# Kernel tuning notes

Measured on AMD Instinct MI355X. Metric: run time of the kernel, lower is better.

The kernel has to match this reference:

```python
import jax, jax.numpy as jnp
import numpy as np

B, E, D, H, A = 65536, 16, 256, 64, 18  # batch, n_subpolicies, emb_dim, hidden, n_actions


def setup_inputs() -> dict:
    key = jax.random.key(0)
    ks = jax.random.split(key, 16)
    s = lambda k, sh: jax.random.normal(k, sh, dtype=jnp.float32) * 0.05
    return dict(
        obs=s(ks[0], (B, D)),
        h=s(ks[1], (B, D)),
        c=s(ks[2], (B, D)),
        idxs=jax.random.randint(ks[3], (B,), 0, E, dtype=jnp.int32),
        # Observer: LSTMCell(D, D) params (torch layout: [4D, D] with i,f,g,o gate order)
        W_ih=s(ks[4], (4 * D, D)), W_hh=s(ks[5], (4 * D, D)),
        b_ih=s(ks[6], (4 * D,)), b_hh=s(ks[7], (4 * D,)),
        # Stacked SubPolicy actor params: Linear(D,64)-Tanh-Linear(64,A)
        Wa1=s(ks[8], (E, D, H)), ba1=s(ks[9], (E, H)),
        Wa2=s(ks[10], (E, H, A)), ba2=s(ks[11], (E, A)),
        # Stacked SubPolicy critic params: Linear(D,64)-Tanh-Linear(64,1)
        Wc1=s(ks[12], (E, D, H)), bc1=s(ks[13], (E, H)),
        Wc2=s(ks[14], (E, H, 1)), bc2=s(ks[15], (E, 1)),
    )


def reference(obs, h, c, idxs, W_ih, W_hh, b_ih, b_hh,
              Wa1, ba1, Wa2, ba2, Wc1, bc1, Wc2, bc2):
    # ---- Observer: single LSTMCell step ----
    gates = obs @ W_ih.T + b_ih + h @ W_hh.T + b_hh          # [B, 4D]
    gi, gf, gg, go = jnp.split(gates, 4, axis=1)
    i = jax.nn.sigmoid(gi); f = jax.nn.sigmoid(gf); o = jax.nn.sigmoid(go)
    c_new = f * c + i * jnp.tanh(gg)                          # [B, D]
    h_new = o * jnp.tanh(c_new)                               # [B, D]

    # ---- Expert dispatch: evaluate all tiny subpolicy MLPs, select per sample ----
    # (mathematically identical to the per-sample routing loop in forward_sub)
    ha = jnp.tanh(jnp.einsum('bd,edh->beh', h_new, Wa1) + ba1)        # [B, E, H]
    logits_all = jnp.einsum('beh,eha->bea', ha, Wa2) + ba2            # [B, E, A]
    hc = jnp.tanh(jnp.einsum('bd,edh->beh', h_new, Wc1) + bc1)        # [B, E, H]
    vals_all = (jnp.einsum('beh,eho->beo', hc, Wc2) + bc2)[..., 0]    # [B, E]

    b = jnp.arange(h_new.shape[0])
    logits = logits_all[b, idxs]                                       # [B, A]
    values = vals_all[b, idxs]                                         # [B]
    return (h_new, c_new, logits, values)
```

## Files before the change

kernel.cpp:

```cpp
#include <hip/hip_runtime.h>
#include <hip/hip_bf16.h>
#include <math.h>

#define NB 65536
#define ND 256
#define NE 16
#define NH 64
#define NA 18

typedef __bf16 bf16;
typedef __bf16 bf16x4 __attribute__((ext_vector_type(4)));
typedef __bf16 bf16x8 __attribute__((ext_vector_type(8)));
typedef float  f32x4  __attribute__((ext_vector_type(4)));

#define OFF_WCAT 0u
#define OFF_BCAT 1048576u
#define OFF_PW1  1052672u
#define OFF_B1   2101248u
#define OFF_CUR  2109440u
#define OFF_PERM 2109504u

__device__ __forceinline__ float rcp_(float x) { return __builtin_amdgcn_rcpf(x); }
__device__ __forceinline__ float sigm_(float x) {
    return rcp_(1.f + __expf(-x));
}
__device__ __forceinline__ float tanh_(float x) {
    float cl = fminf(fmaxf(x, -15.f), 15.f);
    float e = __expf(2.f * cl);
    return (e - 1.f) * rcp_(e + 1.f);
}

__global__ void k_prep1(const float* __restrict__ W_ih, const float* __restrict__ W_hh,
                        const float* __restrict__ b_ih, const float* __restrict__ b_hh,
                        char* __restrict__ ws) {
    int t = blockIdx.x * 256 + threadIdx.x;
    bf16* Wcat = (bf16*)(ws + OFF_WCAT);
    int kc = t & 63, col = t >> 6;
    int k = kc * 8;
    const float* src = (k < 256) ? (W_ih + (size_t)col * 256 + k)
                                 : (W_hh + (size_t)col * 256 + (k - 256));
    float4 v0 = *(const float4*)(src);
    float4 v1 = *(const float4*)(src + 4);
    bf16x8 o;
    o[0] = (bf16)v0.x; o[1] = (bf16)v0.y; o[2] = (bf16)v0.z; o[3] = (bf16)v0.w;
    o[4] = (bf16)v1.x; o[5] = (bf16)v1.y; o[6] = (bf16)v1.z; o[7] = (bf16)v1.w;
    *(bf16x8*)(Wcat + ((size_t)kc * 1024 + col) * 8) = o;
    if (t < 1024) ((float*)(ws + OFF_BCAT))[t] = b_ih[t] + b_hh[t];
    if (t < 16)   ((int*)(ws + OFF_CUR))[t] = t * 65536;
}

__global__ void k_prep2(const float* __restrict__ Wa1, const float* __restrict__ Wc1,
                        const float* __restrict__ ba1, const float* __restrict__ bc1,
                        char* __restrict__ ws) {
    int t = blockIdx.x * 256 + threadIdx.x;
    bf16* PW1 = (bf16*)(ws + OFF_PW1);
    int col = t & 127, kc = (t >> 7) & 31, e = t >> 12;
    bf16x8 o;
#pragma unroll
    for (int j = 0; j < 8; ++j) {
        int k = kc * 8 + j;
        float v = (col < 64) ? Wa1[((size_t)e * 256 + k) * 64 + col]
                             : Wc1[((size_t)e * 256 + k) * 64 + (col - 64)];
        o[j] = (bf16)v;
    }
    *(bf16x8*)(PW1 + (((size_t)e * 32 + kc) * 128 + col) * 8) = o;
    if (t < 2048) {
        int e2 = t >> 7, c = t & 127;
        ((float*)(ws + OFF_B1))[t] = (c < 64) ? ba1[e2 * 64 + c] : bc1[e2 * 64 + (c - 64)];
    }
}

__global__ void k_scatter(const int* __restrict__ idxs, char* __restrict__ ws) {
    __shared__ int lh[16], lbase[16];
    int t = threadIdx.x;
    int i = blockIdx.x * 256 + t;
    if (t < 16) lh[t] = 0;
    __syncthreads();
    int e = idxs[i];
    int r = atomicAdd(&lh[e], 1);
    __syncthreads();
    int* cur = (int*)(ws + OFF_CUR);
    if (t < 16) lbase[t] = atomicAdd(&cur[t], lh[t]);
    __syncthreads();
    ((int*)(ws + OFF_PERM))[lbase[e] + r] = i;
}

__global__ __launch_bounds__(512, 4) void k_lstm(
    const float* __restrict__ obs, const float* __restrict__ hin,
    const float* __restrict__ cin, const float* __restrict__ bcat,
    const bf16* __restrict__ Wcat,
    float* __restrict__ hout, float* __restrict__ cout) {
    __shared__ alignas(16) char Alds[65536];
    const int tid  = threadIdx.x;
    const int wave = tid >> 6, lane = tid & 63;
    const int lr = lane & 15, lk = lane >> 4;
    const int rb = blockIdx.x & 1023, chalf = blockIdx.x >> 10;
    const int row0 = rb * 64;
    const int colc = chalf * 128 + wave * 16 + lr;

    {
        int sr = tid >> 3, j = tid & 7;
        const float* baseO = obs + (size_t)(row0 + sr) * 256;
        const float* baseH = hin + (size_t)(row0 + sr) * 256;
#pragma unroll
        for (int s = 0; s < 8; ++s) {
            int kc = s * 8 + j;
            const float* sp = (s < 4) ? (baseO + kc * 8) : (baseH + (kc - 32) * 8);
            float4 v0 = *(const float4*)sp;
            float4 v1 = *(const float4*)(sp + 4);
            bf16x8 o;
            o[0] = (bf16)v0.x; o[1] = (bf16)v0.y; o[2] = (bf16)v0.z; o[3] = (bf16)v0.w;
            o[4] = (bf16)v1.x; o[5] = (bf16)v1.y; o[6] = (bf16)v1.z; o[7] = (bf16)v1.w;
            *(bf16x8*)(Alds + kc * 1024 + (((sr ^ (kc & 7))) * 16)) = o;
        }
    }
    __syncthreads();

    int offE[4], offO[4];
#pragma unroll
    for (int m = 0; m < 4; ++m) {
        int R = m * 16 + lr;
        offE[m] = lk * 1024 + ((R ^ lk) * 16);
        offO[m] = lk * 1024 + ((R ^ (lk + 4)) * 16);
    }

    f32x4 acc[4][4];
#pragma unroll
    for (int m = 0; m < 4; ++m)
#pragma unroll
        for (int g = 0; g < 4; ++g)
#pragma unroll
            for (int r = 0; r < 4; ++r) acc[m][g][r] = 0.f;

    const bf16* pB = Wcat + ((size_t)lk * 1024 + colc) * 8;

#pragma unroll
    for (int kf = 0; kf < 16; ++kf) {
        const char* Ab = Alds + kf * 4096;
        bf16x8 a0, a1, a2, a3;
        if (kf & 1) {
            a0 = *(const bf16x8*)(Ab + offO[0]);
            a1 = *(const bf16x8*)(Ab + offO[1]);
            a2 = *(const bf16x8*)(Ab + offO[2]);
            a3 = *(const bf16x8*)(Ab + offO[3]);
        } else {
            a0 = *(const bf16x8*)(Ab + offE[0]);
            a1 = *(const bf16x8*)(Ab + offE[1]);
            a2 = *(const bf16x8*)(Ab + offE[2]);
            a3 = *(const bf16x8*)(Ab + offE[3]);
        }
        const bf16* pBk = pB + (size_t)kf * 4 * 1024 * 8;
        bf16x8 b0 = *(const bf16x8*)(pBk);
        bf16x8 b1 = *(const bf16x8*)(pBk + 256 * 8);
        bf16x8 b2 = *(const bf16x8*)(pBk + 512 * 8);
        bf16x8 b3 = *(const bf16x8*)(pBk + 768 * 8);
        acc[0][0] = __builtin_amdgcn_mfma_f32_16x16x32_bf16(a0, b0, acc[0][0], 0, 0, 0);
        acc[0][1] = __builtin_amdgcn_mfma_f32_16x16x32_bf16(a0, b1, acc[0][1], 0, 0, 0);
        acc[0][2] = __builtin_amdgcn_mfma_f32_16x16x32_bf16(a0, b2, acc[0][2], 0, 0, 0);
        acc[0][3] = __builtin_amdgcn_mfma_f32_16x16x32_bf16(a0, b3, acc[0][3], 0, 0, 0);
        acc[1][0] = __builtin_amdgcn_mfma_f32_16x16x32_bf16(a1, b0, acc[1][0], 0, 0, 0);
        acc[1][1] = __builtin_amdgcn_mfma_f32_16x16x32_bf16(a1, b1, acc[1][1], 0, 0, 0);
        acc[1][2] = __builtin_amdgcn_mfma_f32_16x16x32_bf16(a1, b2, acc[1][2], 0, 0, 0);
        acc[1][3] = __builtin_amdgcn_mfma_f32_16x16x32_bf16(a1, b3, acc[1][3], 0, 0, 0);
        acc[2][0] = __builtin_amdgcn_mfma_f32_16x16x32_bf16(a2, b0, acc[2][0], 0, 0, 0);
        acc[2][1] = __builtin_amdgcn_mfma_f32_16x16x32_bf16(a2, b1, acc[2][1], 0, 0, 0);
        acc[2][2] = __builtin_amdgcn_mfma_f32_16x16x32_bf16(a2, b2, acc[2][2], 0, 0, 0);
        acc[2][3] = __builtin_amdgcn_mfma_f32_16x16x32_bf16(a2, b3, acc[2][3], 0, 0, 0);
        acc[3][0] = __builtin_amdgcn_mfma_f32_16x16x32_bf16(a3, b0, acc[3][0], 0, 0, 0);
        acc[3][1] = __builtin_amdgcn_mfma_f32_16x16x32_bf16(a3, b1, acc[3][1], 0, 0, 0);
        acc[3][2] = __builtin_amdgcn_mfma_f32_16x16x32_bf16(a3, b2, acc[3][2], 0, 0, 0);
        acc[3][3] = __builtin_amdgcn_mfma_f32_16x16x32_bf16(a3, b3, acc[3][3], 0, 0, 0);
    }

    float bi = bcat[colc], bf_ = bcat[256 + colc], bg = bcat[512 + colc], bo = bcat[768 + colc];
#pragma unroll
    for (int m = 0; m < 4; ++m) {
#pragma unroll
        for (int r = 0; r < 4; ++r) {
            int row = row0 + m * 16 + lk * 4 + r;
            float gi = acc[m][0][r] + bi;
            float gf = acc[m][1][r] + bf_;
            float gg = acc[m][2][r] + bg;
            float go = acc[m][3][r] + bo;
            float iv = sigm_(gi), fv = sigm_(gf), gv = tanh_(gg), ov = sigm_(go);
            float co = cin[(size_t)row * 256 + colc];
            float cn = fv * co + iv * gv;
            float hn = ov * tanh_(cn);
            cout[(size_t)row * 256 + colc] = cn;
            hout[(size_t)row * 256 + colc] = hn;
        }
    }
}

__global__ __launch_bounds__(256) void k_expert(
    const float* __restrict__ Wa2, const float* __restrict__ ba2,
    const float* __restrict__ Wc2, const float* __restrict__ bc2,
    char* __restrict__ ws, const float* __restrict__ hsrc,
    float* __restrict__ lout, float* __restrict__ vout) {
    const int e = blockIdx.y;
    const int* cur = (const int*)(ws + OFF_CUR);
    int cnt = cur[e] - e * 65536;
    int r0 = blockIdx.x * 64;
    if (r0 >= cnt) return;
    int nr = min(64, cnt - r0);
    const int* permE = (const int*)(ws + OFF_PERM) + (size_t)e * 65536 + r0;

    __shared__ int rows_s[64];
    __shared__ alignas(16) char smem[128 * 66 * 4];
    bf16*  Alds = (bf16*)smem;
    float* haF  = (float*)smem;

    int t = threadIdx.x;
    if (t < 64) rows_s[t] = permE[(t < nr) ? t : 0];
    __syncthreads();

    {
        int rowi = t >> 2, q = t & 3;
        const float* hp = hsrc + (size_t)rows_s[rowi] * 256;
#pragma unroll
        for (int s = 0; s < 8; ++s) {
            int kc = s * 4 + q;
            float4 v0 = *(const float4*)(hp + kc * 8);
            float4 v1 = *(const float4*)(hp + kc * 8 + 4);
            bf16x8 o;
            o[0] = (bf16)v0.x; o[1] = (bf16)v0.y; o[2] = (bf16)v0.z; o[3] = (bf16)v0.w;
            o[4] = (bf16)v1.x; o[5] = (bf16)v1.y; o[6] = (bf16)v1.z; o[7] = (bf16)v1.w;
            *(bf16x8*)(Alds + ((size_t)kc * 64 + rowi) * 8) = o;
        }
    }
    __syncthreads();

    const bf16* PW1 = (const bf16*)(ws + OFF_PW1) + (size_t)e * 32 * 128 * 8;
    const float* b1 = (const float*)(ws + OFF_B1) + e * 128;
    int wave = t >> 6, lane = t & 63, lr = lane & 15, lk = lane >> 4;

    f32x4 acc[4][2];
#pragma unroll
    for (int m = 0; m < 4; ++m)
#pragma unroll
        for (int n = 0; n < 2; ++n)
#pragma unroll
            for (int r = 0; r < 4; ++r) acc[m][n][r] = 0.f;

#pragma unroll
    for (int kf = 0; kf < 8; ++kf) {
        bf16x8 a[4], bb[2];
#pragma unroll
        for (int m = 0; m < 4; ++m)
            a[m] = *(const bf16x8*)(Alds + (((kf * 4 + lk) * 64) + (m * 16 + lr)) * 8);
#pragma unroll
        for (int n = 0; n < 2; ++n) {
            int colh = wave * 32 + n * 16 + lr;
            int kc = kf * 4 + lk;
            bb[n] = *(const bf16x8*)(PW1 + ((size_t)kc * 128 + colh) * 8);
        }
#pragma unroll
        for (int m = 0; m < 4; ++m)
#pragma unroll
            for (int n = 0; n < 2; ++n)
                acc[m][n] = __builtin_amdgcn_mfma_f32_16x16x32_bf16(a[m], bb[n], acc[m][n], 0, 0, 0);
    }
    __syncthreads();

#pragma unroll
    for (int m = 0; m < 4; ++m)
#pragma unroll
        for (int n = 0; n < 2; ++n) {
            int colh = wave * 32 + n * 16 + lr;
            float bbv = b1[colh];
#pragma unroll
            for (int r = 0; r < 4; ++r) {
                int row = m * 16 + lk * 4 + r;
                haF[colh * 66 + row] = tanh_(acc[m][n][r] + bbv);
            }
        }
    __syncthreads();

    int row = t & 63;
    int grow = rows_s[row];
    bool valid = row < nr;
#pragma unroll
    for (int p = 0; p < 5; ++p) {
        int aI = p * 4 + (t >> 6);
        if (aI < NA) {
            float s = ba2[e * NA + aI];
            for (int hh = 0; hh < 64; ++hh)
                s += haF[hh * 66 + row] * Wa2[((size_t)e * 64 + hh) * NA + aI];
            if (valid) lout[(size_t)grow * NA + aI] = s;
        }
    }
    if (t < 64) {
        float s = bc2[e];
        for (int hh = 0; hh < 64; ++hh)
            s += haF[(64 + hh) * 66 + row] * Wc2[e * 64 + hh];
        if (valid) vout[grow] = s;
    }
}

extern "C" void kernel_launch(void* const* d_in, const int* in_sizes, int n_in,
                              void* d_out, int out_size, void* d_ws, size_t ws_size,
                              hipStream_t stream) {
    const float* obs  = (const float*)d_in[0];
    const float* h    = (const float*)d_in[1];
    const float* c    = (const float*)d_in[2];
    const int*   idxs = (const int*)d_in[3];
    const float* W_ih = (const float*)d_in[4];
    const float* W_hh = (const float*)d_in[5];
    const float* b_ih = (const float*)d_in[6];
    const float* b_hh = (const float*)d_in[7];
    const float* Wa1  = (const float*)d_in[8];
    const float* ba1  = (const float*)d_in[9];
    const float* Wa2  = (const float*)d_in[10];
    const float* ba2  = (const float*)d_in[11];
    const float* Wc1  = (const float*)d_in[12];
    const float* bc1  = (const float*)d_in[13];
    const float* Wc2  = (const float*)d_in[14];
    const float* bc2  = (const float*)d_in[15];

    float* out  = (float*)d_out;
    float* hout = out;
    float* cout = out + (size_t)NB * ND;
    float* lout = out + (size_t)2 * NB * ND;
    float* vout = lout + (size_t)NB * NA;
    char* ws = (char*)d_ws;

    k_prep1<<<dim3(256), dim3(256), 0, stream>>>(W_ih, W_hh, b_ih, b_hh, ws);
    k_prep2<<<dim3(256), dim3(256), 0, stream>>>(Wa1, Wc1, ba1, bc1, ws);
    k_scatter<<<dim3(256), dim3(256), 0, stream>>>(idxs, ws);
    k_lstm<<<dim3(2048), dim3(512), 0, stream>>>(
        obs, h, c, (const float*)(ws + OFF_BCAT), (const bf16*)(ws + OFF_WCAT), hout, cout);
    k_expert<<<dim3(1024, 16), dim3(256), 0, stream>>>(
        Wa2, ba2, Wc2, bc2, ws, hout, lout, vout);
}
```

Baseline: 211.2 us.

## Compute all 1024 gate columns per LSTM block and double-buffer B loads

The LSTM kernel now has each 64-row block compute all 256 hidden columns (1024 gate outputs) instead of splitting columns across two blocks. This halves the grid and avoids staging and converting the obs/h rows to bf16 twice. Each wave now holds 32 accumulators for 8 column tiles, and the weight fragments for the next k-step are prefetched into a second register buffer. Launch bounds drop to 2 blocks per CU to fit the larger register footprint, which cuts occupancy.

```diff
diff --git a/kernel.cpp b/kernel.cpp
--- a/kernel.cpp
+++ b/kernel.cpp
@@ -85,7 +85,7 @@
     ((int*)(ws + OFF_PERM))[lbase[e] + r] = i;
 }
 
-__global__ __launch_bounds__(512, 4) void k_lstm(
+__global__ __launch_bounds__(512, 2) void k_lstm(
     const float* __restrict__ obs, const float* __restrict__ hin,
     const float* __restrict__ cin, const float* __restrict__ bcat,
     const bf16* __restrict__ Wcat,
@@ -94,9 +94,7 @@
     const int tid  = threadIdx.x;
     const int wave = tid >> 6, lane = tid & 63;
     const int lr = lane & 15, lk = lane >> 4;
-    const int rb = blockIdx.x & 1023, chalf = blockIdx.x >> 10;
-    const int row0 = rb * 64;
-    const int colc = chalf * 128 + wave * 16 + lr;
+    const int row0 = blockIdx.x * 64;
 
     {
         int sr = tid >> 3, j = tid & 7;
@@ -124,70 +122,79 @@
         offO[m] = lk * 1024 + ((R ^ (lk + 4)) * 16);
     }
 
-    f32x4 acc[4][4];
+    f32x4 acc[4][8];
 #pragma unroll
     for (int m = 0; m < 4; ++m)
 #pragma unroll
-        for (int g = 0; g < 4; ++g)
-#pragma unroll
-            for (int r = 0; r < 4; ++r) acc[m][g][r] = 0.f;
-
-    const bf16* pB = Wcat + ((size_t)lk * 1024 + colc) * 8;
-
-#pragma unroll
-    for (int kf = 0; kf < 16; ++kf) {
-        const char* Ab = Alds + kf * 4096;
-        bf16x8 a0, a1, a2, a3;
-        if (kf & 1) {
-            a0 = *(const bf16x8*)(Ab + offO[0]);
-            a1 = *(const bf16x8*)(Ab + offO[1]);
-            a2 = *(const bf16x8*)(Ab + offO[2]);
-            a3 = *(const bf16x8*)(Ab + offO[3]);
-        } else {
-            a0 = *(const bf16x8*)(Ab + offE[0]);
-            a1 = *(const bf16x8*)(Ab + offE[1]);
-            a2 = *(const bf16x8*)(Ab + offE[2]);
-            a3 = *(const bf16x8*)(Ab + offE[3]);
-        }
-        const bf16* pBk = pB + (size_t)kf * 4 * 1024 * 8;
-        bf16x8 b0 = *(const bf16x8*)(pBk);
-        bf16x8 b1 = *(const bf16x8*)(pBk + 256 * 8);
-        bf16x8 b2 = *(const bf16x8*)(pBk + 512 * 8);
-        bf16x8 b3 = *(const bf16x8*)(pBk + 768 * 8);
-        acc[0][0] = __builtin_amdgcn_mfma_f32_16x16x32_bf16(a0, b0, acc[0][0], 0, 0, 0);
-        acc[0][1] = __builtin_amdgcn_mfma_f32_16x16x32_bf16(a0, b1, acc[0][1], 0, 0, 0);
-        acc[0][2] = __builtin_amdgcn_mfma_f32_16x16x32_bf16(a0, b2, acc[0][2], 0, 0, 0);
-        acc[0][3] = __builtin_amdgcn_mfma_f32_16x16x32_bf16(a0, b3, acc[0][3], 0, 0, 0);
-        acc[1][0] = __builtin_amdgcn_mfma_f32_16x16x32_bf16(a1, b0, acc[1][0], 0, 0, 0);
-        acc[1][1] = __builtin_amdgcn_mfma_f32_16x16x32_bf16(a1, b1, acc[1][1], 0, 0, 0);
-        acc[1][2] = __builtin_amdgcn_mfma_f32_16x16x32_bf16(a1, b2, acc[1][2], 0, 0, 0);
-        acc[1][3] = __builtin_amdgcn_mfma_f32_16x16x32_bf16(a1, b3, acc[1][3], 0, 0, 0);
-        acc[2][0] = __builtin_amdgcn_mfma_f32_16x16x32_bf16(a2, b0, acc[2][0], 0, 0, 0);
-        acc[2][1] = __builtin_amdgcn_mfma_f32_16x16x32_bf16(a2, b1, acc[2][1], 0, 0, 0);
-        acc[2][2] = __builtin_amdgcn_mfma_f32_16x16x32_bf16(a2, b2, acc[2][2], 0, 0, 0);
-        acc[2][3] = __builtin_amdgcn_mfma_f32_16x16x32_bf16(a2, b3, acc[2][3], 0, 0, 0);
-        acc[3][0] = __builtin_amdgcn_mfma_f32_16x16x32_bf16(a3, b0, acc[3][0], 0, 0, 0);
-        acc[3][1] = __builtin_amdgcn_mfma_f32_16x16x32_bf16(a3, b1, acc[3][1], 0, 0, 0);
-        acc[3][2] = __builtin_amdgcn_mfma_f32_16x16x32_bf16(a3, b2, acc[3][2], 0, 0, 0);
-        acc[3][3] = __builtin_amdgcn_mfma_f32_16x16x32_bf16(a3, b3, acc[3][3], 0, 0, 0);
-    }
-
-    float bi = bcat[colc], bf_ = bcat[256 + colc], bg = bcat[512 + colc], bo = bcat[768 + colc];
-#pragma unroll
-    for (int m = 0; m < 4; ++m) {
-#pragma unroll
-        for (int r = 0; r < 4; ++r) {
-            int row = row0 + m * 16 + lk * 4 + r;
-            float gi = acc[m][0][r] + bi;
-            float gf = acc[m][1][r] + bf_;
-            float gg = acc[m][2][r] + bg;
-            float go = acc[m][3][r] + bo;
-            float iv = sigm_(gi), fv = sigm_(gf), gv = tanh_(gg), ov = sigm_(go);
-            float co = cin[(size_t)row * 256 + colc];
-            float cn = fv * co + iv * gv;
-            float hn = ov * tanh_(cn);
-            cout[(size_t)row * 256 + colc] = cn;
-            hout[(size_t)row * 256 + colc] = hn;
+        for (int n = 0; n < 8; ++n)
+#pragma unroll
+            for (int r = 0; r < 4; ++r) acc[m][n][r] = 0.f;
+
+    const bf16* pB = Wcat + ((size_t)lk * 1024 + wave * 32 + lr) * 8;
+#define BOFF(g, j) ((g) * 2048 + (j) * 128)
+
+    bf16x8 B0[8], B1[8];
+#define LOADB(dst, kf)                                                        \
+    {                                                                         \
+        const bf16* p_ = pB + (size_t)(kf) * 32768;                           \
+        dst[0] = *(const bf16x8*)(p_ + BOFF(0, 0));                           \
+        dst[1] = *(const bf16x8*)(p_ + BOFF(0, 1));                           \
+        dst[2] = *(const bf16x8*)(p_ + BOFF(1, 0));                           \
+        dst[3] = *(const bf16x8*)(p_ + BOFF(1, 1));                           \
+        dst[4] = *(const bf16x8*)(p_ + BOFF(2, 0));                           \
+        dst[5] = *(const bf16x8*)(p_ + BOFF(2, 1));                           \
+        dst[6] = *(const bf16x8*)(p_ + BOFF(3, 0));                           \
+        dst[7] = *(const bf16x8*)(p_ + BOFF(3, 1));                           \
+    }
+
+#define STEP(kf, BCUR, BNXT, OFFA)                                            \
+    {                                                                         \
+        if ((kf) < 15) LOADB(BNXT, (kf) + 1);                                 \
+        const char* Ab_ = Alds + (kf) * 4096;                                 \
+        bf16x8 a0 = *(const bf16x8*)(Ab_ + OFFA[0]);                          \
+        bf16x8 a1 = *(const bf16x8*)(Ab_ + OFFA[1]);                          \
+        bf16x8 a2 = *(const bf16x8*)(Ab_ + OFFA[2]);                          \
+        bf16x8 a3 = *(const bf16x8*)(Ab_ + OFFA[3]);                          \
+        _Pragma("unroll")                                                     \
+        for (int n = 0; n < 8; ++n) {                                         \
+            acc[0][n] = __builtin_amdgcn_mfma_f32_16x16x32_bf16(a0, BCUR[n], acc[0][n], 0, 0, 0); \
+            acc[1][n] = __builtin_amdgcn_mfma_f32_16x16x32_bf16(a1, BCUR[n], acc[1][n], 0, 0, 0); \
+            acc[2][n] = __builtin_amdgcn_mfma_f32_16x16x32_bf16(a2, BCUR[n], acc[2][n], 0, 0, 0); \
+            acc[3][n] = __builtin_amdgcn_mfma_f32_16x16x32_bf16(a3, BCUR[n], acc[3][n], 0, 0, 0); \
+        }                                                                     \
+    }
+
+    LOADB(B0, 0);
+#pragma unroll
+    for (int kk = 0; kk < 8; ++kk) {
+        STEP(kk * 2,     B0, B1, offE);
+        STEP(kk * 2 + 1, B1, B0, offO);
+    }
+#undef STEP
+#undef LOADB
+#undef BOFF
+
+    const int colb = wave * 32 + lr;
+#pragma unroll
+    for (int j = 0; j < 2; ++j) {
+        int col = colb + j * 16;
+        float bi = bcat[col], bf_ = bcat[256 + col], bg = bcat[512 + col], bo = bcat[768 + col];
+#pragma unroll
+        for (int m = 0; m < 4; ++m) {
+#pragma unroll
+            for (int r = 0; r < 4; ++r) {
+                int row = row0 + m * 16 + lk * 4 + r;
+                float gi = acc[m][0 * 2 + j][r] + bi;
+                float gf = acc[m][1 * 2 + j][r] + bf_;
+                float gg = acc[m][2 * 2 + j][r] + bg;
+                float go = acc[m][3 * 2 + j][r] + bo;
+                float iv = sigm_(gi), fv = sigm_(gf), gv = tanh_(gg), ov = sigm_(go);
+                float co = cin[(size_t)row * 256 + col];
+                float cn = fv * co + iv * gv;
+                float hn = ov * tanh_(cn);
+                cout[(size_t)row * 256 + col] = cn;
+                hout[(size_t)row * 256 + col] = hn;
+            }
         }
     }
 }
@@ -327,7 +334,7 @@
     k_prep1<<<dim3(256), dim3(256), 0, stream>>>(W_ih, W_hh, b_ih, b_hh, ws);
     k_prep2<<<dim3(256), dim3(256), 0, stream>>>(Wa1, Wc1, ba1, bc1, ws);
     k_scatter<<<dim3(256), dim3(256), 0, stream>>>(idxs, ws);
-    k_lstm<<<dim3(2048), dim3(512), 0, stream>>>(
+    k_lstm<<<dim3(1024), dim3(512), 0, stream>>>(
         obs, h, c, (const float*)(ws + OFF_BCAT), (const bf16*)(ws + OFF_WCAT), hout, cout);
     k_expert<<<dim3(1024, 16), dim3(256), 0, stream>>>(
         Wa2, ba2, Wc2, bc2, ws, hout, lout, vout);
```

After: 286.6 us. 35.7% more time.

## Double-buffer LSTM GEMM K-loop with direct global-to-LDS weight staging

Applied to the files above, without the earlier changes.

Rewrites the LSTM gate GEMM so that it streams K in eight steps through double-buffered LDS. Weight tiles are staged with global_load_lds into a pre-tiled layout, which k_prep1 now produces, and the next activation tile is loaded and converted while the current one is computed. Blocks shrink to 256 threads covering 64 gate columns, which doubles the grid, and the c input is prefetched during the last step. The goal is to overlap the global loads with the MFMAs and cut per-block LDS use, at the cost of reading the activations once per column block (four times instead of twice) and adding more barriers.

```diff
diff --git a/kernel.cpp b/kernel.cpp
--- a/kernel.cpp
+++ b/kernel.cpp
@@ -21,30 +21,38 @@
 #define OFF_PERM 2109504u
 
 __device__ __forceinline__ float rcp_(float x) { return __builtin_amdgcn_rcpf(x); }
-__device__ __forceinline__ float sigm_(float x) {
-    return rcp_(1.f + __expf(-x));
-}
+__device__ __forceinline__ float sigm_(float x) { return rcp_(1.f + __expf(-x)); }
 __device__ __forceinline__ float tanh_(float x) {
     float cl = fminf(fmaxf(x, -15.f), 15.f);
     float e = __expf(2.f * cl);
     return (e - 1.f) * rcp_(e + 1.f);
 }
 
+__device__ __forceinline__ void gl2lds16(const void* g, void* l) {
+    __builtin_amdgcn_global_load_lds(
+        (const __attribute__((address_space(1))) unsigned int*)g,
+        (__attribute__((address_space(3))) unsigned int*)l, 16, 0, 0);
+}
+
 __global__ void k_prep1(const float* __restrict__ W_ih, const float* __restrict__ W_hh,
                         const float* __restrict__ b_ih, const float* __restrict__ b_hh,
                         char* __restrict__ ws) {
     int t = blockIdx.x * 256 + threadIdx.x;
-    bf16* Wcat = (bf16*)(ws + OFF_WCAT);
-    int kc = t & 63, col = t >> 6;
-    int k = kc * 8;
-    const float* src = (k < 256) ? (W_ih + (size_t)col * 256 + k)
-                                 : (W_hh + (size_t)col * 256 + (k - 256));
+    int kstep = t >> 13, rem = t & 8191;
+    int cb = rem >> 11, u = rem & 2047;
+    int hi = u >> 8, lo = u & 255;
+    int kf = hi >> 2, g = hi & 3;
+    int colw = lo >> 2, lk = lo & 3;
+    int col = g * 256 + cb * 64 + colw;
+    int k0 = kstep * 64 + (kf * 4 + lk) * 8;
+    const float* src = (k0 < 256) ? (W_ih + (size_t)col * 256 + k0)
+                                  : (W_hh + (size_t)col * 256 + (k0 - 256));
     float4 v0 = *(const float4*)(src);
     float4 v1 = *(const float4*)(src + 4);
     bf16x8 o;
     o[0] = (bf16)v0.x; o[1] = (bf16)v0.y; o[2] = (bf16)v0.z; o[3] = (bf16)v0.w;
     o[4] = (bf16)v1.x; o[5] = (bf16)v1.y; o[6] = (bf16)v1.z; o[7] = (bf16)v1.w;
-    *(bf16x8*)(Wcat + ((size_t)kc * 1024 + col) * 8) = o;
+    *(bf16x8*)((bf16*)(ws + OFF_WCAT) + (size_t)t * 8) = o;
     if (t < 1024) ((float*)(ws + OFF_BCAT))[t] = b_ih[t] + b_hh[t];
     if (t < 16)   ((int*)(ws + OFF_CUR))[t] = t * 65536;
 }
@@ -85,44 +93,33 @@
     ((int*)(ws + OFF_PERM))[lbase[e] + r] = i;
 }
 
-__global__ __launch_bounds__(512, 4) void k_lstm(
+__global__ __launch_bounds__(256, 2) void k_lstm(
     const float* __restrict__ obs, const float* __restrict__ hin,
     const float* __restrict__ cin, const float* __restrict__ bcat,
-    const bf16* __restrict__ Wcat,
+    const char* __restrict__ wcat,
     float* __restrict__ hout, float* __restrict__ cout) {
-    __shared__ alignas(16) char Alds[65536];
+    __shared__ alignas(16) char Abuf[2][8192];
+    __shared__ alignas(16) char Bbuf[2][32768];
     const int tid  = threadIdx.x;
-    const int wave = tid >> 6, lane = tid & 63;
+    const int w = tid >> 6, lane = tid & 63;
     const int lr = lane & 15, lk = lane >> 4;
-    const int rb = blockIdx.x & 1023, chalf = blockIdx.x >> 10;
+    const int rb = blockIdx.x & 1023, cb = blockIdx.x >> 10;
     const int row0 = rb * 64;
-    const int colc = chalf * 128 + wave * 16 + lr;
-
-    {
-        int sr = tid >> 3, j = tid & 7;
-        const float* baseO = obs + (size_t)(row0 + sr) * 256;
-        const float* baseH = hin + (size_t)(row0 + sr) * 256;
-#pragma unroll
-        for (int s = 0; s < 8; ++s) {
-            int kc = s * 8 + j;
-            const float* sp = (s < 4) ? (baseO + kc * 8) : (baseH + (kc - 32) * 8);
-            float4 v0 = *(const float4*)sp;
-            float4 v1 = *(const float4*)(sp + 4);
-            bf16x8 o;
-            o[0] = (bf16)v0.x; o[1] = (bf16)v0.y; o[2] = (bf16)v0.z; o[3] = (bf16)v0.w;
-            o[4] = (bf16)v1.x; o[5] = (bf16)v1.y; o[6] = (bf16)v1.z; o[7] = (bf16)v1.w;
-            *(bf16x8*)(Alds + kc * 1024 + (((sr ^ (kc & 7))) * 16)) = o;
-        }
-    }
-    __syncthreads();
+    const int colc = cb * 64 + w * 16 + lr;
+    const int srw = tid >> 3, sj = tid & 7;
+
+    const char* WcatBlk = wcat + (size_t)cb * 32768;
+    const float* baseO0 = obs + (size_t)(row0 + srw) * 256 + sj * 8;
+    const float* baseH0 = hin + (size_t)(row0 + srw) * 256 + sj * 8;
 
     int offE[4], offO[4];
 #pragma unroll
     for (int m = 0; m < 4; ++m) {
         int R = m * 16 + lr;
         offE[m] = lk * 1024 + ((R ^ lk) * 16);
-        offO[m] = lk * 1024 + ((R ^ (lk + 4)) * 16);
-    }
+        offO[m] = (lk + 4) * 1024 + ((R ^ (lk + 4)) * 16);
+    }
+    const int bBase = (w * 16 + lr) * 64 + lk * 16;
 
     f32x4 acc[4][4];
 #pragma unroll
@@ -132,45 +129,97 @@
 #pragma unroll
             for (int r = 0; r < 4; ++r) acc[m][g][r] = 0.f;
 
-    const bf16* pB = Wcat + ((size_t)lk * 1024 + colc) * 8;
-
-#pragma unroll
-    for (int kf = 0; kf < 16; ++kf) {
-        const char* Ab = Alds + kf * 4096;
-        bf16x8 a0, a1, a2, a3;
-        if (kf & 1) {
-            a0 = *(const bf16x8*)(Ab + offO[0]);
-            a1 = *(const bf16x8*)(Ab + offO[1]);
-            a2 = *(const bf16x8*)(Ab + offO[2]);
-            a3 = *(const bf16x8*)(Ab + offO[3]);
+#define STAGE_B(bi, ks)                                                      \
+    {                                                                        \
+        const char* srcB_ = WcatBlk + (size_t)(ks) * 131072;                 \
+        _Pragma("unroll")                                                    \
+        for (int i_ = 0; i_ < 8; ++i_) {                                     \
+            int so_ = (w * 8 + i_) * 1024;                                   \
+            gl2lds16(srcB_ + so_ + lane * 16, &Bbuf[bi][so_]);               \
+        }                                                                    \
+    }
+#define LOAD_A(ks)                                                           \
+    {                                                                        \
+        const float* s0_ = ((ks) < 4) ? (baseO0 + (ks) * 64)                 \
+                                      : (baseH0 + ((ks) - 4) * 64);          \
+        na0 = *(const float4*)(s0_);                                         \
+        na1 = *(const float4*)(s0_ + 4);                                     \
+        nb0 = *(const float4*)(s0_ + 32 * 256);                              \
+        nb1 = *(const float4*)(s0_ + 32 * 256 + 4);                          \
+    }
+#define WRITE_A(bi)                                                          \
+    {                                                                        \
+        bf16x8 oa_, ob_;                                                     \
+        oa_[0] = (bf16)na0.x; oa_[1] = (bf16)na0.y; oa_[2] = (bf16)na0.z;    \
+        oa_[3] = (bf16)na0.w; oa_[4] = (bf16)na1.x; oa_[5] = (bf16)na1.y;    \
+        oa_[6] = (bf16)na1.z; oa_[7] = (bf16)na1.w;                          \
+        ob_[0] = (bf16)nb0.x; ob_[1] = (bf16)nb0.y; ob_[2] = (bf16)nb0.z;    \
+        ob_[3] = (bf16)nb0.w; ob_[4] = (bf16)nb1.x; ob_[5] = (bf16)nb1.y;    \
+        ob_[6] = (bf16)nb1.z; ob_[7] = (bf16)nb1.w;                          \
+        *(bf16x8*)(&Abuf[bi][sj * 1024 + ((srw ^ sj) * 16)]) = oa_;          \
+        *(bf16x8*)(&Abuf[bi][sj * 1024 + (((srw + 32) ^ sj) * 16)]) = ob_;   \
+    }
+
+    {
+        float4 na0, na1, nb0, nb1;
+        STAGE_B(0, 0);
+        LOAD_A(0);
+        WRITE_A(0);
+    }
+    __syncthreads();
+
+    float cpre[16];
+
+#pragma unroll
+    for (int t = 0; t < 8; ++t) {
+        const int cur = t & 1;
+        float4 na0, na1, nb0, nb1;
+        if (t < 7) {
+            STAGE_B(cur ^ 1, t + 1);
+            LOAD_A(t + 1);
         } else {
-            a0 = *(const bf16x8*)(Ab + offE[0]);
-            a1 = *(const bf16x8*)(Ab + offE[1]);
-            a2 = *(const bf16x8*)(Ab + offE[2]);
-            a3 = *(const bf16x8*)(Ab + offE[3]);
-        }
-        const bf16* pBk = pB + (size_t)kf * 4 * 1024 * 8;
-        bf16x8 b0 = *(const bf16x8*)(pBk);
-        bf16x8 b1 = *(const bf16x8*)(pBk + 256 * 8);
-        bf16x8 b2 = *(const bf16x8*)(pBk + 512 * 8);
-        bf16x8 b3 = *(const bf16x8*)(pBk + 768 * 8);
-        acc[0][0] = __builtin_amdgcn_mfma_f32_16x16x32_bf16(a0, b0, acc[0][0], 0, 0, 0);
-        acc[0][1] = __builtin_amdgcn_mfma_f32_16x16x32_bf16(a0, b1, acc[0][1], 0, 0, 0);
-        acc[0][2] = __builtin_amdgcn_mfma_f32_16x16x32_bf16(a0, b2, acc[0][2], 0, 0, 0);
-        acc[0][3] = __builtin_amdgcn_mfma_f32_16x16x32_bf16(a0, b3, acc[0][3], 0, 0, 0);
-        acc[1][0] = __builtin_amdgcn_mfma_f32_16x16x32_bf16(a1, b0, acc[1][0], 0, 0, 0);
-        acc[1][1] = __builtin_amdgcn_mfma_f32_16x16x32_bf16(a1, b1, acc[1][1], 0, 0, 0);
-        acc[1][2] = __builtin_amdgcn_mfma_f32_16x16x32_bf16(a1, b2, acc[1][2], 0, 0, 0);
-        acc[1][3] = __builtin_amdgcn_mfma_f32_16x16x32_bf16(a1, b3, acc[1][3], 0, 0, 0);
-        acc[2][0] = __builtin_amdgcn_mfma_f32_16x16x32_bf16(a2, b0, acc[2][0], 0, 0, 0);
-        acc[2][1] = __builtin_amdgcn_mfma_f32_16x16x32_bf16(a2, b1, acc[2][1], 0, 0, 0);
-        acc[2][2] = __builtin_amdgcn_mfma_f32_16x16x32_bf16(a2, b2, acc[2][2], 0, 0, 0);
-        acc[2][3] = __builtin_amdgcn_mfma_f32_16x16x32_bf16(a2, b3, acc[2][3], 0, 0, 0);
-        acc[3][0] = __builtin_amdgcn_mfma_f32_16x16x32_bf16(a3, b0, acc[3][0], 0, 0, 0);
-        acc[3][1] = __builtin_amdgcn_mfma_f32_16x16x32_bf16(a3, b1, acc[3][1], 0, 0, 0);
-        acc[3][2] = __builtin_amdgcn_mfma_f32_16x16x32_bf16(a3, b2, acc[3][2], 0, 0, 0);
-        acc[3][3] = __builtin_amdgcn_mfma_f32_16x16x32_bf16(a3, b3, acc[3][3], 0, 0, 0);
-    }
+#pragma unroll
+            for (int m = 0; m < 4; ++m)
+#pragma unroll
+                for (int r = 0; r < 4; ++r)
+                    cpre[m * 4 + r] = cin[(size_t)(row0 + m * 16 + lk * 4 + r) * 256 + colc];
+        }
+#pragma unroll
+        for (int kf = 0; kf < 2; ++kf) {
+            const char* Ab = Abuf[cur];
+            const int* offA = kf ? offO : offE;
+            bf16x8 a0 = *(const bf16x8*)(Ab + offA[0]);
+            bf16x8 a1 = *(const bf16x8*)(Ab + offA[1]);
+            bf16x8 a2 = *(const bf16x8*)(Ab + offA[2]);
+            bf16x8 a3 = *(const bf16x8*)(Ab + offA[3]);
+            const char* Bb = Bbuf[cur] + kf * 16384 + bBase;
+            bf16x8 b0 = *(const bf16x8*)(Bb);
+            bf16x8 b1 = *(const bf16x8*)(Bb + 4096);
+            bf16x8 b2 = *(const bf16x8*)(Bb + 8192);
+            bf16x8 b3 = *(const bf16x8*)(Bb + 12288);
+            acc[0][0] = __builtin_amdgcn_mfma_f32_16x16x32_bf16(a0, b0, acc[0][0], 0, 0, 0);
+            acc[1][0] = __builtin_amdgcn_mfma_f32_16x16x32_bf16(a1, b0, acc[1][0], 0, 0, 0);
+            acc[2][0] = __builtin_amdgcn_mfma_f32_16x16x32_bf16(a2, b0, acc[2][0], 0, 0, 0);
+            acc[3][0] = __builtin_amdgcn_mfma_f32_16x16x32_bf16(a3, b0, acc[3][0], 0, 0, 0);
+            acc[0][1] = __builtin_amdgcn_mfma_f32_16x16x32_bf16(a0, b1, acc[0][1], 0, 0, 0);
+            acc[1][1] = __builtin_amdgcn_mfma_f32_16x16x32_bf16(a1, b1, acc[1][1], 0, 0, 0);
+            acc[2][1] = __builtin_amdgcn_mfma_f32_16x16x32_bf16(a2, b1, acc[2][1], 0, 0, 0);
+            acc[3][1] = __builtin_amdgcn_mfma_f32_16x16x32_bf16(a3, b1, acc[3][1], 0, 0, 0);
+            acc[0][2] = __builtin_amdgcn_mfma_f32_16x16x32_bf16(a0, b2, acc[0][2], 0, 0, 0);
+            acc[1][2] = __builtin_amdgcn_mfma_f32_16x16x32_bf16(a1, b2, acc[1][2], 0, 0, 0);
+            acc[2][2] = __builtin_amdgcn_mfma_f32_16x16x32_bf16(a2, b2, acc[2][2], 0, 0, 0);
+            acc[3][2] = __builtin_amdgcn_mfma_f32_16x16x32_bf16(a3, b2, acc[3][2], 0, 0, 0);
+            acc[0][3] = __builtin_amdgcn_mfma_f32_16x16x32_bf16(a0, b3, acc[0][3], 0, 0, 0);
+            acc[1][3] = __builtin_amdgcn_mfma_f32_16x16x32_bf16(a1, b3, acc[1][3], 0, 0, 0);
+            acc[2][3] = __builtin_amdgcn_mfma_f32_16x16x32_bf16(a2, b3, acc[2][3], 0, 0, 0);
+            acc[3][3] = __builtin_amdgcn_mfma_f32_16x16x32_bf16(a3, b3, acc[3][3], 0, 0, 0);
+        }
+        if (t < 7) WRITE_A(cur ^ 1);
+        __syncthreads();
+    }
+#undef STAGE_B
+#undef LOAD_A
+#undef WRITE_A
 
     float bi = bcat[colc], bf_ = bcat[256 + colc], bg = bcat[512 + colc], bo = bcat[768 + colc];
 #pragma unroll
@@ -183,8 +232,7 @@
             float gg = acc[m][2][r] + bg;
             float go = acc[m][3][r] + bo;
             float iv = sigm_(gi), fv = sigm_(gf), gv = tanh_(gg), ov = sigm_(go);
-            float co = cin[(size_t)row * 256 + colc];
-            float cn = fv * co + iv * gv;
+            float cn = fv * cpre[m * 4 + r] + iv * gv;
             float hn = ov * tanh_(cn);
             cout[(size_t)row * 256 + colc] = cn;
             hout[(size_t)row * 256 + colc] = hn;
@@ -327,8 +375,8 @@
     k_prep1<<<dim3(256), dim3(256), 0, stream>>>(W_ih, W_hh, b_ih, b_hh, ws);
     k_prep2<<<dim3(256), dim3(256), 0, stream>>>(Wa1, Wc1, ba1, bc1, ws);
     k_scatter<<<dim3(256), dim3(256), 0, stream>>>(idxs, ws);
-    k_lstm<<<dim3(2048), dim3(512), 0, stream>>>(
-        obs, h, c, (const float*)(ws + OFF_BCAT), (const bf16*)(ws + OFF_WCAT), hout, cout);
+    k_lstm<<<dim3(4096), dim3(256), 0, stream>>>(
+        obs, h, c, (const float*)(ws + OFF_BCAT), (const char*)(ws + OFF_WCAT), hout, cout);
     k_expert<<<dim3(1024, 16), dim3(256), 0, stream>>>(
         Wa2, ba2, Wc2, bc2, ws, hout, lout, vout);
 }
```

After: 222.8 us. 1.06x slower.
